# Optimization experiments

Measured on AMD Instinct MI355X. Metric: run time of the kernel, lower is better.

## Reference

```python
import jax, jax.numpy as jnp
import numpy as np

N = 100000   # nodes
E = 3200000  # edges (avg degree 32)
IN_DIM = 512
HIDDEN = 128
NUM_CLASSES = 64
NLAYERS = 2


def _xavier(key, fan_in, fan_out):
    b = math_bound = (6.0 / (fan_in + fan_out)) ** 0.5
    return jax.random.uniform(key, (fan_in, fan_out), jnp.float32, -b, b)


def setup_inputs() -> dict:
    key = jax.random.key(0)
    k1, k2, k3, k4, k5, k6 = jax.random.split(key, 6)
    features = jax.random.normal(k1, (N, IN_DIM), dtype=jnp.float32)
    edge_src = jax.random.randint(k2, (E,), 0, N, dtype=jnp.int32)
    edge_dst = jax.random.randint(k3, (E,), 0, N, dtype=jnp.int32)
    edge_val = jax.random.uniform(k4, (E,), dtype=jnp.float32)  # normalized adj values
    W0 = _xavier(k5, IN_DIM, HIDDEN)
    W1 = _xavier(k6, HIDDEN, NUM_CLASSES)
    return {
        "features": features,
        "W0": W0,
        "W1": W1,
        "edge_val": edge_val,
        "edge_src": edge_src,
        "edge_dst": edge_dst,
    }


def _spmm(edge_src, edge_dst, edge_val, x):
    # z[dst] += val * x[src]  -- sparse adj @ dense features
    return jax.ops.segment_sum(edge_val[:, None] * x[edge_src], edge_dst,
                               num_segments=N)


def reference(features, W0, W1, edge_val, edge_src, edge_dst):
    # Dense NN phase: GEMM + ReLU between layers, no ReLU after the last.
    h = jax.nn.relu(features @ W0)  # [N, HIDDEN]
    h = h @ W1                      # [N, NUM_CLASSES]
    # Graph phase: nlayers repeated SpMM aggregations with the full adjacency.
    # (world_size=1 => split/gather and feature-dim padding are identity.)
    for _ in range(NLAYERS):
        h = _spmm(edge_src, edge_dst, edge_val, h)
    return h
```

## Files before the change

kernel.cpp:

```cpp
#include <hip/hip_runtime.h>
#include <hip/hip_bf16.h>

#define NNODES 100000
#define NEDGES 3200000
#define INDIM  512
#define HID    128
#define NCLS   64

#define NBUCK  256
#define NPB    391
#define NCAP   (NBUCK * NPB)
#define BCAP   16384
#define CHUNK  4096
#define NCHUNKB ((NEDGES + CHUNK - 1) / CHUNK)

typedef __bf16 bf16x8 __attribute__((ext_vector_type(8)));
typedef __bf16 bf16x4 __attribute__((ext_vector_type(4)));
typedef float  f32x4  __attribute__((ext_vector_type(4)));

#define HPAD 136

__global__ __launch_bounds__(256)
void k_count_wcvt(const int* __restrict__ dst, int* __restrict__ gcnt,
                  int* __restrict__ my_base,
                  const float* __restrict__ W0, const float* __restrict__ W1,
                  __bf16* __restrict__ W0P, __bf16* __restrict__ W1P) {
  const int t = threadIdx.x;
  if (blockIdx.x == NCHUNKB) {
    for (int i = t; i < 65536; i += 256) {
      const int c = i >> 3, j = i & 7;
      const int ln = c & 63, tt = (c >> 6) & 7, kk = c >> 9;
      const int row = tt * 16 + (ln & 15);
      const int k   = kk * 32 + (ln >> 4) * 8 + j;
      W0P[i] = (__bf16)W0[k * HID + row];
    }
    for (int i = t; i < 8192; i += 256) {
      const int c = i >> 3, j = i & 7;
      const int ln = c & 63, tt = (c >> 6) & 3, kk = c >> 8;
      const int row = tt * 16 + (ln & 15);
      const int k   = kk * 32 + (ln >> 4) * 8 + j;
      W1P[i] = (__bf16)W1[k * NCLS + row];
    }
    return;
  }
  __shared__ int cnt[NBUCK];
  cnt[t] = 0;
  __syncthreads();
  const int base = blockIdx.x * CHUNK;
#pragma unroll
  for (int j = 0; j < CHUNK / 1024; ++j) {
    const int e = base + (j * 256 + t) * 4;
    if (e < NEDGES) {
      const int4 d = *(const int4*)&dst[e];
      atomicAdd(&cnt[(unsigned)d.x / NPB], 1);
      atomicAdd(&cnt[(unsigned)d.y / NPB], 1);
      atomicAdd(&cnt[(unsigned)d.z / NPB], 1);
      atomicAdd(&cnt[(unsigned)d.w / NPB], 1);
    }
  }
  __syncthreads();
  my_base[blockIdx.x * NBUCK + t] = atomicAdd(&gcnt[t], cnt[t]);
}

__global__ void kA_bscan(const int* __restrict__ gcnt, int* __restrict__ bbase) {
  __shared__ int s[256];
  const int t = threadIdx.x;
  const int v = gcnt[t];
  s[t] = v;
  __syncthreads();
  for (int off = 1; off < 256; off <<= 1) {
    int x = (t >= off) ? s[t - off] : 0;
    __syncthreads();
    s[t] += x;
    __syncthreads();
  }
  bbase[t] = s[t] - v;
  if (t == 255) bbase[256] = s[255];
}

__global__ __launch_bounds__(256, 4)
void k_scatter_gemm(const int* __restrict__ dst, const int* __restrict__ src,
                    const float* __restrict__ val, const int* __restrict__ bbase,
                    const int* __restrict__ my_base, int2* __restrict__ bsv,
                    const float* __restrict__ feat, const __bf16* __restrict__ W0P,
                    const __bf16* __restrict__ W1P, __bf16* __restrict__ h1b) {
  __shared__ __align__(16) char smem[64 * HPAD * 2];
  const int tid = threadIdx.x;

  if (blockIdx.x < NCHUNKB) {
    int* cur = (int*)smem;
    cur[tid] = bbase[tid] + my_base[blockIdx.x * NBUCK + tid];
    __syncthreads();
    const int base = blockIdx.x * CHUNK;
#pragma unroll
    for (int j = 0; j < CHUNK / 1024; ++j) {
      const int e = base + (j * 256 + tid) * 4;
      if (e < NEDGES) {
        const int4   d  = *(const int4*)&dst[e];
        const int4   sc = *(const int4*)&src[e];
        const float4 vv = *(const float4*)&val[e];
        int p, b, ld;
        b = (unsigned)d.x / NPB; ld = d.x - b * NPB;
        p = atomicAdd(&cur[b], 1);
        bsv[p] = make_int2(sc.x | (ld << 17), __float_as_int(vv.x));
        b = (unsigned)d.y / NPB; ld = d.y - b * NPB;
        p = atomicAdd(&cur[b], 1);
        bsv[p] = make_int2(sc.y | (ld << 17), __float_as_int(vv.y));
        b = (unsigned)d.z / NPB; ld = d.z - b * NPB;
        p = atomicAdd(&cur[b], 1);
        bsv[p] = make_int2(sc.z | (ld << 17), __float_as_int(vv.z));
        b = (unsigned)d.w / NPB; ld = d.w - b * NPB;
        p = atomicAdd(&cur[b], 1);
        bsv[p] = make_int2(sc.w | (ld << 17), __float_as_int(vv.w));
      }
    }
    return;
  }

  __bf16* h0s = (__bf16*)smem;

  const int wave = tid >> 6;
  const int lane = tid & 63;
  const int q    = lane >> 4;
  const int l16  = lane & 15;
  const int rb   = (blockIdx.x - NCHUNKB) * 64;

  int row = rb + wave * 16 + l16;
  if (row >= NNODES) row = NNODES - 1;
  const float4* __restrict__ arow4 =
      (const float4*)(feat + (size_t)row * INDIM);

  f32x4 acc[8];
#pragma unroll
  for (int t = 0; t < 8; ++t) acc[t] = (f32x4){0.f, 0.f, 0.f, 0.f};

  float4 pa0 = arow4[q * 2],     pa1 = arow4[q * 2 + 1];
  float4 qa0 = arow4[8 + q * 2], qa1 = arow4[8 + q * 2 + 1];

#pragma unroll 2
  for (int kk = 0; kk < INDIM / 32; ++kk) {
    float4 na0 = pa0, na1 = pa1;
    if (kk < INDIM / 32 - 2) {
      na0 = arow4[(kk + 2) * 8 + q * 2];
      na1 = arow4[(kk + 2) * 8 + q * 2 + 1];
    }
    bf16x8 aF;
    aF[0] = (__bf16)pa0.x; aF[1] = (__bf16)pa0.y; aF[2] = (__bf16)pa0.z; aF[3] = (__bf16)pa0.w;
    aF[4] = (__bf16)pa1.x; aF[5] = (__bf16)pa1.y; aF[6] = (__bf16)pa1.z; aF[7] = (__bf16)pa1.w;
#pragma unroll
    for (int t = 0; t < 8; ++t) {
      const bf16x8 bF = *(const bf16x8*)&W0P[(size_t)(((kk * 8 + t) * 64 + lane) * 8)];
      acc[t] = __builtin_amdgcn_mfma_f32_16x16x32_bf16(aF, bF, acc[t], 0, 0, 0);
    }
    pa0 = qa0; pa1 = qa1;
    qa0 = na0; qa1 = na1;
  }

#pragma unroll
  for (int t = 0; t < 8; ++t) {
#pragma unroll
    for (int j = 0; j < 4; ++j) {
      float v = acc[t][j];
      v = v > 0.f ? v : 0.f;
      h0s[(wave * 16 + q * 4 + j) * HPAD + t * 16 + l16] = (__bf16)v;
    }
  }

  f32x4 acc2[4];
#pragma unroll
  for (int t = 0; t < 4; ++t) acc2[t] = (f32x4){0.f, 0.f, 0.f, 0.f};
#pragma unroll
  for (int kk = 0; kk < HID / 32; ++kk) {
    const bf16x8 aF = *(const bf16x8*)&h0s[(wave * 16 + l16) * HPAD + kk * 32 + q * 8];
#pragma unroll
    for (int t = 0; t < 4; ++t) {
      const bf16x8 bF = *(const bf16x8*)&W1P[(size_t)(((kk * 4 + t) * 64 + lane) * 8)];
      acc2[t] = __builtin_amdgcn_mfma_f32_16x16x32_bf16(aF, bF, acc2[t], 0, 0, 0);
    }
  }

#pragma unroll
  for (int t = 0; t < 4; ++t) {
#pragma unroll
    for (int j = 0; j < 4; ++j) {
      const int grow = rb + wave * 16 + q * 4 + j;
      if (grow < NNODES)
        h1b[(size_t)grow * NCLS + t * 16 + l16] = (__bf16)acc2[t][j];
    }
  }
}

__global__ __launch_bounds__(1024)
void kB3(const int2* __restrict__ bsv, const int* __restrict__ bbase,
         int2* __restrict__ rowinfo, int2* __restrict__ ecsr) {
  __shared__ int dl[NPB];
  __shared__ int cur[NPB];
  __shared__ int s[512];
  const int t = threadIdx.x;
  const int b = blockIdx.x;
  const int nb = b * NPB;
  for (int i = t; i < NPB; i += 1024) dl[i] = 0;
  __syncthreads();
  const int beg = bbase[b], end = bbase[b + 1];
  for (int e = beg + t; e < end; e += 1024)
    atomicAdd(&dl[((unsigned)bsv[e].x) >> 17], 1);
  __syncthreads();
  int d = 0, pd = 0;
  if (t < 512) {
    d  = (t < NPB) ? dl[t] : 0;
    pd = (d + 7) & ~7;
    s[t] = pd;
  }
  __syncthreads();
  for (int off = 1; off < 512; off <<= 1) {
    int x = 0;
    if (t < 512 && t >= off) x = s[t - off];
    __syncthreads();
    if (t < 512) s[t] += x;
    __syncthreads();
  }
  const int gb = b * BCAP;
  const int2 z2 = make_int2(0, 0);
  if (t < NPB) {
    const int excl = s[t] - pd;
    const int c = gb + excl;
    cur[t] = c;
    if (nb + t < NNODES) rowinfo[nb + t] = make_int2(c, pd);
    for (int k = d; k < pd; ++k) ecsr[c + k] = z2;
  }
  __syncthreads();
  for (int e = beg + t; e < end; e += 1024) {
    const int2 sv = bsv[e];
    const int ld = ((unsigned)sv.x) >> 17;
    const int p = atomicAdd(&cur[ld], 1);
    ecsr[p] = make_int2(sv.x & 0x1FFFF, sv.y);
  }
}

template <typename OUT_T>
__global__ __launch_bounds__(256, 4)
void k_spmm(const int2* __restrict__ rowinfo, const int2* __restrict__ ecsr,
            const __bf16* __restrict__ x, OUT_T* __restrict__ y) {
  const int wid  = (blockIdx.x * 256 + threadIdx.x) >> 6;
  const int lane = threadIdx.x & 63;
  const int g    = lane >> 4;
  const int l16  = lane & 15;
  const int row  = wid * 4 + g;
  const int c0   = l16 * 4;
  const int2 ri  = rowinfo[row];
  const int base = ri.x, pdeg = ri.y;
  f32x4 acc = (f32x4){0.f, 0.f, 0.f, 0.f};
  for (int j = 0; j < pdeg; j += 8) {
    const int4 m0 = *(const int4*)&ecsr[base + j];
    const int4 m1 = *(const int4*)&ecsr[base + j + 2];
    const int4 m2 = *(const int4*)&ecsr[base + j + 4];
    const int4 m3 = *(const int4*)&ecsr[base + j + 6];
    const bf16x4 x0 = *(const bf16x4*)&x[(size_t)m0.x * NCLS + c0];
    const bf16x4 x1 = *(const bf16x4*)&x[(size_t)m0.z * NCLS + c0];
    const bf16x4 x2 = *(const bf16x4*)&x[(size_t)m1.x * NCLS + c0];
    const bf16x4 x3 = *(const bf16x4*)&x[(size_t)m1.z * NCLS + c0];
    const bf16x4 x4 = *(const bf16x4*)&x[(size_t)m2.x * NCLS + c0];
    const bf16x4 x5 = *(const bf16x4*)&x[(size_t)m2.z * NCLS + c0];
    const bf16x4 x6 = *(const bf16x4*)&x[(size_t)m3.x * NCLS + c0];
    const bf16x4 x7 = *(const bf16x4*)&x[(size_t)m3.z * NCLS + c0];
    const float v0 = __int_as_float(m0.y), v1 = __int_as_float(m0.w);
    const float v2 = __int_as_float(m1.y), v3 = __int_as_float(m1.w);
    const float v4 = __int_as_float(m2.y), v5 = __int_as_float(m2.w);
    const float v6 = __int_as_float(m3.y), v7 = __int_as_float(m3.w);
#pragma unroll
    for (int i = 0; i < 4; ++i) {
      acc[i] += v0 * (float)x0[i];
      acc[i] += v1 * (float)x1[i];
      acc[i] += v2 * (float)x2[i];
      acc[i] += v3 * (float)x3[i];
      acc[i] += v4 * (float)x4[i];
      acc[i] += v5 * (float)x5[i];
      acc[i] += v6 * (float)x6[i];
      acc[i] += v7 * (float)x7[i];
    }
  }
  if constexpr (sizeof(OUT_T) == 4) {
    float4 o;
    o.x = acc[0]; o.y = acc[1]; o.z = acc[2]; o.w = acc[3];
    *(float4*)&y[(size_t)row * NCLS + c0] = o;
  } else {
    bf16x4 o;
    o[0] = (__bf16)acc[0]; o[1] = (__bf16)acc[1];
    o[2] = (__bf16)acc[2]; o[3] = (__bf16)acc[3];
    *(bf16x4*)&y[(size_t)row * NCLS + c0] = o;
  }
}

extern "C" void kernel_launch(void* const* d_in, const int* in_sizes, int n_in,
                              void* d_out, int out_size, void* d_ws, size_t ws_size,
                              hipStream_t stream) {
  const float* feat = (const float*)d_in[0];
  const float* W0   = (const float*)d_in[1];
  const float* W1   = (const float*)d_in[2];
  const float* eval = (const float*)d_in[3];
  const int*   esrc = (const int*)d_in[4];
  const int*   edst = (const int*)d_in[5];
  float* out = (float*)d_out;

  char* p = (char*)d_ws;
  int2*   ecsr    = (int2*)p;   p += (size_t)NBUCK * BCAP * 8;
  int2*   rowinfo = (int2*)p;   p += (size_t)NCAP * 8;
  int*    gcnt    = (int*)p;    p += 1024;
  int*    bbase   = (int*)p;    p += 2048;
  __bf16* W0P     = (__bf16*)p; p += 131072;
  __bf16* W1P     = (__bf16*)p; p += 16384;
  __bf16* h1b     = (__bf16*)p; p += 12800000;
  __bf16* h2b     = (__bf16*)p; p += 12800000;
  int*    my_base = (int*)h2b;
  int2*   bsv     = (int2*)d_out;

  hipMemsetAsync(gcnt, 0, NBUCK * sizeof(int), stream);
  k_count_wcvt <<<NCHUNKB + 1, 256, 0, stream>>>(edst, gcnt, my_base,
                                                 W0, W1, W0P, W1P);
  kA_bscan     <<<1, 256, 0, stream>>>(gcnt, bbase);
  k_scatter_gemm<<<NCHUNKB + (NNODES + 63) / 64, 256, 0, stream>>>(
      edst, esrc, eval, bbase, my_base, bsv, feat, W0P, W1P, h1b);
  kB3          <<<NBUCK, 1024, 0, stream>>>(bsv, bbase, rowinfo, ecsr);

  k_spmm<__bf16><<<NNODES / 16, 256, 0, stream>>>(rowinfo, ecsr, h1b, h2b);
  k_spmm<float> <<<NNODES / 16, 256, 0, stream>>>(rowinfo, ecsr, h2b, out);

  (void)in_sizes; (void)n_in; (void)out_size; (void)ws_size;
}
```

Baseline: 569.8 us.

## Build CSR directly with per-node global atomics instead of two-pass bucketing

```diff
diff --git a/kernel.cpp b/kernel.cpp
--- a/kernel.cpp
+++ b/kernel.cpp
@@ -7,12 +7,11 @@
 #define HID    128
 #define NCLS   64
 
-#define NBUCK  256
-#define NPB    391
-#define NCAP   (NBUCK * NPB)
-#define BCAP   16384
 #define CHUNK  4096
 #define NCHUNKB ((NEDGES + CHUNK - 1) / CHUNK)
+
+#define ECSR_CAP (4u << 20)
+#define NSCAN    ((NNODES + 511) / 512)
 
 typedef __bf16 bf16x8 __attribute__((ext_vector_type(8)));
 typedef __bf16 bf16x4 __attribute__((ext_vector_type(4)));
@@ -21,8 +20,7 @@
 #define HPAD 136
 
 __global__ __launch_bounds__(256)
-void k_count_wcvt(const int* __restrict__ dst, int* __restrict__ gcnt,
-                  int* __restrict__ my_base,
+void k_count_wcvt(const int* __restrict__ dst, int* __restrict__ deg,
                   const float* __restrict__ W0, const float* __restrict__ W1,
                   __bf16* __restrict__ W0P, __bf16* __restrict__ W1P) {
   const int t = threadIdx.x;
@@ -43,54 +41,56 @@
     }
     return;
   }
-  __shared__ int cnt[NBUCK];
-  cnt[t] = 0;
-  __syncthreads();
   const int base = blockIdx.x * CHUNK;
 #pragma unroll
   for (int j = 0; j < CHUNK / 1024; ++j) {
     const int e = base + (j * 256 + t) * 4;
     if (e < NEDGES) {
       const int4 d = *(const int4*)&dst[e];
-      atomicAdd(&cnt[(unsigned)d.x / NPB], 1);
-      atomicAdd(&cnt[(unsigned)d.y / NPB], 1);
-      atomicAdd(&cnt[(unsigned)d.z / NPB], 1);
-      atomicAdd(&cnt[(unsigned)d.w / NPB], 1);
-    }
-  }
+      atomicAdd(&deg[d.x], 1);
+      atomicAdd(&deg[d.y], 1);
+      atomicAdd(&deg[d.z], 1);
+      atomicAdd(&deg[d.w], 1);
+    }
+  }
+}
+
+__global__ __launch_bounds__(512)
+void k_lscan(const int* __restrict__ deg, int* __restrict__ galloc,
+             int2* __restrict__ rowinfo, int* __restrict__ cur) {
+  __shared__ int s[512];
+  __shared__ int segbase;
+  const int t = threadIdx.x;
+  const int n = blockIdx.x * 512 + t;
+  const int d  = (n < NNODES) ? deg[n] : 0;
+  const int pd = (d + 7) & ~7;
+  s[t] = pd;
   __syncthreads();
-  my_base[blockIdx.x * NBUCK + t] = atomicAdd(&gcnt[t], cnt[t]);
-}
-
-__global__ void kA_bscan(const int* __restrict__ gcnt, int* __restrict__ bbase) {
-  __shared__ int s[256];
-  const int t = threadIdx.x;
-  const int v = gcnt[t];
-  s[t] = v;
-  __syncthreads();
-  for (int off = 1; off < 256; off <<= 1) {
+  for (int off = 1; off < 512; off <<= 1) {
     int x = (t >= off) ? s[t - off] : 0;
     __syncthreads();
     s[t] += x;
     __syncthreads();
   }
-  bbase[t] = s[t] - v;
-  if (t == 255) bbase[256] = s[255];
+  if (t == 511) segbase = atomicAdd(galloc, s[511]);
+  __syncthreads();
+  if (n < NNODES) {
+    const int st = segbase + s[t] - pd;
+    rowinfo[n] = make_int2(st, pd);
+    cur[n] = st;
+  }
 }
 
 __global__ __launch_bounds__(256, 4)
 void k_scatter_gemm(const int* __restrict__ dst, const int* __restrict__ src,
-                    const float* __restrict__ val, const int* __restrict__ bbase,
-                    const int* __restrict__ my_base, int2* __restrict__ bsv,
+                    const float* __restrict__ val, int* __restrict__ cur,
+                    int2* __restrict__ ecsr,
                     const float* __restrict__ feat, const __bf16* __restrict__ W0P,
                     const __bf16* __restrict__ W1P, __bf16* __restrict__ h1b) {
   __shared__ __align__(16) char smem[64 * HPAD * 2];
   const int tid = threadIdx.x;
 
   if (blockIdx.x < NCHUNKB) {
-    int* cur = (int*)smem;
-    cur[tid] = bbase[tid] + my_base[blockIdx.x * NBUCK + tid];
-    __syncthreads();
     const int base = blockIdx.x * CHUNK;
 #pragma unroll
     for (int j = 0; j < CHUNK / 1024; ++j) {
@@ -99,19 +99,15 @@
         const int4   d  = *(const int4*)&dst[e];
         const int4   sc = *(const int4*)&src[e];
         const float4 vv = *(const float4*)&val[e];
-        int p, b, ld;
-        b = (unsigned)d.x / NPB; ld = d.x - b * NPB;
-        p = atomicAdd(&cur[b], 1);
-        bsv[p] = make_int2(sc.x | (ld << 17), __float_as_int(vv.x));
-        b = (unsigned)d.y / NPB; ld = d.y - b * NPB;
-        p = atomicAdd(&cur[b], 1);
-        bsv[p] = make_int2(sc.y | (ld << 17), __float_as_int(vv.y));
-        b = (unsigned)d.z / NPB; ld = d.z - b * NPB;
-        p = atomicAdd(&cur[b], 1);
-        bsv[p] = make_int2(sc.z | (ld << 17), __float_as_int(vv.z));
-        b = (unsigned)d.w / NPB; ld = d.w - b * NPB;
-        p = atomicAdd(&cur[b], 1);
-        bsv[p] = make_int2(sc.w | (ld << 17), __float_as_int(vv.w));
+        int p;
+        p = atomicAdd(&cur[d.x], 1);
+        ecsr[p] = make_int2(sc.x, __float_as_int(vv.x));
+        p = atomicAdd(&cur[d.y], 1);
+        ecsr[p] = make_int2(sc.y, __float_as_int(vv.y));
+        p = atomicAdd(&cur[d.z], 1);
+        ecsr[p] = make_int2(sc.z, __float_as_int(vv.z));
+        p = atomicAdd(&cur[d.w], 1);
+        ecsr[p] = make_int2(sc.w, __float_as_int(vv.w));
       }
     }
     return;
@@ -187,53 +183,6 @@
       if (grow < NNODES)
         h1b[(size_t)grow * NCLS + t * 16 + l16] = (__bf16)acc2[t][j];
     }
-  }
-}
-
-__global__ __launch_bounds__(1024)
-void kB3(const int2* __restrict__ bsv, const int* __restrict__ bbase,
-         int2* __restrict__ rowinfo, int2* __restrict__ ecsr) {
-  __shared__ int dl[NPB];
-  __shared__ int cur[NPB];
-  __shared__ int s[512];
-  const int t = threadIdx.x;
-  const int b = blockIdx.x;
-  const int nb = b * NPB;
-  for (int i = t; i < NPB; i += 1024) dl[i] = 0;
-  __syncthreads();
-  const int beg = bbase[b], end = bbase[b + 1];
-  for (int e = beg + t; e < end; e += 1024)
-    atomicAdd(&dl[((unsigned)bsv[e].x) >> 17], 1);
-  __syncthreads();
-  int d = 0, pd = 0;
-  if (t < 512) {
-    d  = (t < NPB) ? dl[t] : 0;
-    pd = (d + 7) & ~7;
-    s[t] = pd;
-  }
-  __syncthreads();
-  for (int off = 1; off < 512; off <<= 1) {
-    int x = 0;
-    if (t < 512 && t >= off) x = s[t - off];
-    __syncthreads();
-    if (t < 512) s[t] += x;
-    __syncthreads();
-  }
-  const int gb = b * BCAP;
-  const int2 z2 = make_int2(0, 0);
-  if (t < NPB) {
-    const int excl = s[t] - pd;
-    const int c = gb + excl;
-    cur[t] = c;
-    if (nb + t < NNODES) rowinfo[nb + t] = make_int2(c, pd);
-    for (int k = d; k < pd; ++k) ecsr[c + k] = z2;
-  }
-  __syncthreads();
-  for (int e = beg + t; e < end; e += 1024) {
-    const int2 sv = bsv[e];
-    const int ld = ((unsigned)sv.x) >> 17;
-    const int p = atomicAdd(&cur[ld], 1);
-    ecsr[p] = make_int2(sv.x & 0x1FFFF, sv.y);
   }
 }
 
@@ -303,24 +252,21 @@
   float* out = (float*)d_out;
 
   char* p = (char*)d_ws;
-  int2*   ecsr    = (int2*)p;   p += (size_t)NBUCK * BCAP * 8;
-  int2*   rowinfo = (int2*)p;   p += (size_t)NCAP * 8;
-  int*    gcnt    = (int*)p;    p += 1024;
-  int*    bbase   = (int*)p;    p += 2048;
+  int2*   ecsr    = (int2*)p;   p += (size_t)ECSR_CAP * 8;
+  int*    deg     = (int*)p;    p += 401408;
+  int*    galloc  = (int*)p;    p += 64;
+  int*    cur     = (int*)p;    p += 401408;
+  int2*   rowinfo = (int2*)p;   p += 800768;
   __bf16* W0P     = (__bf16*)p; p += 131072;
   __bf16* W1P     = (__bf16*)p; p += 16384;
-  __bf16* h1b     = (__bf16*)p; p += 12800000;
   __bf16* h2b     = (__bf16*)p; p += 12800000;
-  int*    my_base = (int*)h2b;
-  int2*   bsv     = (int2*)d_out;
-
-  hipMemsetAsync(gcnt, 0, NBUCK * sizeof(int), stream);
-  k_count_wcvt <<<NCHUNKB + 1, 256, 0, stream>>>(edst, gcnt, my_base,
-                                                 W0, W1, W0P, W1P);
-  kA_bscan     <<<1, 256, 0, stream>>>(gcnt, bbase);
+  __bf16* h1b     = (__bf16*)d_out;
+
+  hipMemsetAsync(ecsr, 0, (size_t)ECSR_CAP * 8 + 401408 + 64, stream);
+  k_count_wcvt <<<NCHUNKB + 1, 256, 0, stream>>>(edst, deg, W0, W1, W0P, W1P);
+  k_lscan      <<<NSCAN, 512, 0, stream>>>(deg, galloc, rowinfo, cur);
   k_scatter_gemm<<<NCHUNKB + (NNODES + 63) / 64, 256, 0, stream>>>(
-      edst, esrc, eval, bbase, my_base, bsv, feat, W0P, W1P, h1b);
-  kB3          <<<NBUCK, 1024, 0, stream>>>(bsv, bbase, rowinfo, ecsr);
+      edst, esrc, eval, cur, ecsr, feat, W0P, W1P, h1b);
 
   k_spmm<__bf16><<<NNODES / 16, 256, 0, stream>>>(rowinfo, ecsr, h1b, h2b);
   k_spmm<float> <<<NNODES / 16, 256, 0, stream>>>(rowinfo, ecsr, h2b, out);
```

After: 816.3 us. 1.43x slower.
